# Kernel tuning notes

Hardware: AMD Instinct MI355X
Metric: run time of the kernel (lower is better)

Reference implementation:

```python
import jax, jax.numpy as jnp
import numpy as np
from jax.scipy.special import i0

# --- NUFFT adjoint (Kaiser-Bessel gridding) configuration ---
N = 512            # image side (image_shape)
K = 2 * N
M = 200_000        # n_measurements (visibilities)
B = 8              # batch of measurement vectors
J = 6              # gridding kernel width (plan uses (6, 6))
BETA = 2.34 * J


def setup_inputs() -> dict:
    key = jax.random.key(0)
    k1, k2, k3 = jax.random.split(key, 3)
    # uv coordinates in [-pi, pi) radians per pixel (standard NUFFT convention)
    uv = jax.random.uniform(k1, (M, 2), jnp.float32, -np.pi, np.pi)
    y_real = jax.random.normal(k2, (B, M), jnp.float32)
    y_imag = jax.random.normal(k3, (B, M), jnp.float32)
    weights = jnp.ones((M,), jnp.float32)  # measurement_weights
    return {"y_real": y_real, "y_imag": y_imag, "uv": uv, "weights": weights}


def _grid_1d(coord):
    """Per-axis gridding indices and Kaiser-Bessel weights.

    coord: (M,) frequencies in [-pi, pi). Returns idx (M, J) int32 grid
    columns (wrapped mod K) and w (M, J) float32 kernel weights.
    """
    k = coord / (2.0 * np.pi) * K            # grid units, in [-K/2, K/2)
    km = jnp.floor(k - J / 2.0)              # leftmost neighbor base
    j = jnp.arange(1, J + 1, dtype=k.dtype)
    pts = km[:, None] + j                    # (M, J) grid points covered
    d = k[:, None] - pts                     # signed distance, |d| <= J/2
    arg = jnp.maximum(1.0 - (2.0 * d / J) ** 2, 0.0)
    w = i0(BETA * jnp.sqrt(arg)) / i0(jnp.float32(BETA))
    idx = jnp.mod(pts, K).astype(jnp.int32)
    return idx, w.astype(jnp.float32)


def _deapod(n):
    """Gridding-correction (inverse FT of the KB kernel) at image pixels."""
    x = (jnp.arange(n, dtype=jnp.float32) - n / 2.0) / K
    t = BETA ** 2 - (np.pi * J * x) ** 2
    st = jnp.sqrt(jnp.abs(t))
    num = jnp.where(t > 0, jnp.sinh(st), jnp.sin(st))
    return num / jnp.maximum(st, 1e-6)


def reference(y_real, y_imag, uv, weights):
    y = (y_real + 1j * y_imag).astype(jnp.complex64) * weights  # (B, M)

    ix, wx = _grid_1d(uv[:, 0])  # (M, J)
    iy, wy = _grid_1d(uv[:, 1])  # (M, J)

    # Separable 6x6 kernel: outer products per measurement
    flat_idx = (ix[:, :, None] * K + iy[:, None, :]).reshape(-1)        # (M*J*J,)
    w2 = (wx[:, :, None] * wy[:, None, :]).reshape(M, J * J)            # (M, 36)
    vals = (y[:, :, None] * w2[None]).reshape(B, -1)                    # (B, M*36)

    # Scatter-add onto the oversampled grid (duplicate indices accumulate)
    grid = jnp.zeros((B, K * K), jnp.complex64).at[:, flat_idx].add(vals)
    grid = grid.reshape(B, K, K)

    # Unnormalized inverse FFT (adjoint of the forward FFT), shift to center
    img = jnp.fft.fftshift(jnp.fft.ifft2(grid), axes=(-2, -1)) * (K * K)

    # Crop central N x N region and de-apodize
    s = (K - N) // 2
    img_c = jnp.real(img[:, s:s + N, s:s + N])
    apod = _deapod(N)
    return img_c / (apod[:, None] * apod[None, :])
```

## Files before the change

### kernel.cpp

```cpp
#include <hip/hip_runtime.h>
#include <hip/hip_fp16.h>
#include <math.h>

#define KGRID 1024
#define NIMG  512
#define JW    6
#define BETAF 14.04f
#define NB    8
#define NBIN  16384
#define CAP   96

typedef float v2f __attribute__((ext_vector_type(2)));
typedef float v4f __attribute__((ext_vector_type(4)));

__device__ __forceinline__ float i0f_dev(float x) {
    float ax = fabsf(x);
    if (ax < 3.75f) {
        float z = ax * (1.0f / 3.75f);
        z = z * z;
        return 1.0f + z * (3.5156229f + z * (3.0899424f + z * (1.2067492f +
               z * (0.2659732f + z * (0.0360768f + z * 0.0045813f)))));
    } else {
        float z = 3.75f / ax;
        float p = 0.39894228f + z * (0.01328592f + z * (0.00225319f + z * (-0.00157565f +
                  z * (0.00916281f + z * (-0.02057706f + z * (0.02635537f +
                  z * (-0.01647633f + z * 0.00392377f)))))));
        return expf(ax) * rsqrtf(ax) * p;
    }
}

__global__ __launch_bounds__(256) void prep_kernel(
    const float* __restrict__ yr, const float* __restrict__ yi,
    const float* __restrict__ uv, const float* __restrict__ wts,
    float4* __restrict__ yF4, float4* __restrict__ pnt,
    int* __restrict__ cnt, int* __restrict__ list, int M)
{
    int m = (blockIdx.x >> 1) * 256 + threadIdx.x;
    if (m >= M) return;

    float u = uv[2 * m], v = uv[2 * m + 1];
    const float c2g = (float)KGRID / 6.283185307179586f;
    float kx = u * c2g, ky = v * c2g;
    float kmx = floorf(kx - 3.0f), kmy = floorf(ky - 3.0f);
    int x0m = (((int)kmx + 1) + 1024) & 1023;
    int y0m = (((int)kmy + 1) + 1024) & 1023;

    if ((blockIdx.x & 1) == 0) {
        int txA = x0m >> 3, txB = (txA + 1) & 127;
        int tyA = y0m >> 3, tyB = (tyA + 1) & 127;
        bool bx = (x0m & 7) >= 3;
        bool by = (y0m & 7) >= 3;
        int b0 = (txA << 7) | tyA;
        int b1 = (txA << 7) | tyB;
        int b2 = (txB << 7) | tyA;
        int b3 = (txB << 7) | tyB;
        int s0 = atomicAdd(&cnt[b0], 1);
        int s1 = by ? atomicAdd(&cnt[b1], 1) : -1;
        int s2 = bx ? atomicAdd(&cnt[b2], 1) : -1;
        int s3 = (bx && by) ? atomicAdd(&cnt[b3], 1) : -1;
        if ((unsigned)s0 < CAP) list[b0 * CAP + s0] = m;
        if ((unsigned)s1 < CAP) list[b1 * CAP + s1] = m;
        if ((unsigned)s2 < CAP) list[b2 * CAP + s2] = m;
        if ((unsigned)s3 < CAP) list[b3 * CAP + s3] = m;
    } else {
        if (m == 0) {
            float4 z = make_float4(0.f, 0.f, 0.f, 0.f);
            #pragma unroll
            for (int q = 0; q < 4; q++) { pnt[(size_t)M * 4 + q] = z; yF4[(size_t)M * 4 + q] = z; }
        }

        float inv = 1.0f / i0f_dev(BETAF);
        float s2c = inv * inv;
        float sc = wts[m] * s2c;

        float wx[JW], wy[JW];
        #pragma unroll
        for (int j = 0; j < JW; j++) {
            float dx = kx - kmx - 1.0f - (float)j;
            float rx = dx * (1.0f / 3.0f);
            float ax = fmaxf(1.0f - rx * rx, 0.0f);
            wx[j] = i0f_dev(BETAF * sqrtf(ax)) * sc;
            float dy = ky - kmy - 1.0f - (float)j;
            float ry = dy * (1.0f / 3.0f);
            float ay = fmaxf(1.0f - ry * ry, 0.0f);
            wy[j] = i0f_dev(BETAF * sqrtf(ay));
        }

        float4* p = pnt + (size_t)m * 4;
        p[0] = make_float4(wx[0], wx[1], wx[2], wx[3]);
        p[1] = make_float4(wx[4], wx[5], __int_as_float((x0m << 10) | y0m), 0.0f);
        p[2] = make_float4(wy[0], wy[1], wy[2], wy[3]);
        p[3] = make_float4(wy[4], wy[5], 0.0f, 0.0f);

        #pragma unroll
        for (int bp = 0; bp < 4; bp++) {
            int bb = 2 * bp;
            yF4[(size_t)m * 4 + bp] = make_float4(
                yr[(size_t)bb * M + m],       yi[(size_t)bb * M + m],
                yr[(size_t)(bb + 1) * M + m], yi[(size_t)(bb + 1) * M + m]);
        }
    }
}

__global__ __launch_bounds__(256) void grid_tile(
    const float* __restrict__ pnt1, const float4* __restrict__ yF4,
    const int* __restrict__ cnt, const int* __restrict__ list,
    __half2* __restrict__ gH, int M)
{
    int lane = threadIdx.x & 63;
    int wid  = threadIdx.x >> 6;
    int tile = blockIdx.x * 4 + wid;
    int tx0 = (tile >> 7) << 3;
    int ty0 = (tile & 127) << 3;
    int lx = lane >> 3, ly = lane & 7;
    int slot = lane & 15;

    v2f acc[NB];
    #pragma unroll
    for (int b = 0; b < NB; b++) acc[b] = (v2f){0.f, 0.f};

    int n = cnt[tile]; if (n > CAP) n = CAP;
    const int* lst = list + tile * CAP;
    const v4f* yV = (const v4f*)yF4;

    int lv0 = (lane < n) ? lst[lane] : M;
    int lv1 = (64 + lane < n && 64 + lane < CAP) ? lst[64 + lane] : M;

    #define FETCH_M(i) __builtin_amdgcn_readlane(((i) < 64) ? lv0 : lv1, (i) & 63)

    int   mA = FETCH_M(0), mB = FETCH_M(1), mC = FETCH_M(2);
    float pwA = pnt1[(size_t)mA * 16 + slot];
    float pwB = pnt1[(size_t)mB * 16 + slot];
    float pwC = pnt1[(size_t)mC * 16 + slot];
    v4f yA0 = yV[(size_t)mA * 4 + 0], yA1 = yV[(size_t)mA * 4 + 1],
        yA2 = yV[(size_t)mA * 4 + 2], yA3 = yV[(size_t)mA * 4 + 3];
    v4f yB0 = yV[(size_t)mB * 4 + 0], yB1 = yV[(size_t)mB * 4 + 1],
        yB2 = yV[(size_t)mB * 4 + 2], yB3 = yV[(size_t)mB * 4 + 3];
    v4f yC0 = yV[(size_t)mC * 4 + 0], yC1 = yV[(size_t)mC * 4 + 1],
        yC2 = yV[(size_t)mC * 4 + 2], yC3 = yV[(size_t)mC * 4 + 3];

    #define PROC(PW, Y0, Y1, Y2, Y3, IDX)                                          \
    {                                                                              \
        int mN = FETCH_M((IDX) + 3);                                               \
        int pwb = __float_as_int(PW);                                              \
        int meta = __builtin_amdgcn_readlane(pwb, 6);                              \
        int j1 = (tx0 + lx - (meta >> 10)) & 1023;                                 \
        int j2 = (ty0 + ly - (meta & 1023)) & 1023;                                 \
        int i1 = (j1 < 6) ? j1 : 15;                              \
        int i2 = (j2 < 6) ? (j2 + 8) : 14;                        \
        float wx = __int_as_float(__builtin_amdgcn_ds_bpermute(i1 << 2, pwb));     \
        float wy = __int_as_float(__builtin_amdgcn_ds_bpermute(i2 << 2, pwb));     \
        float w = wx * wy;                                                         \
        v2f w2 = {w, w};                                                           \
        acc[0] = __builtin_elementwise_fma(w2, Y0.xy, acc[0]);                     \
        acc[1] = __builtin_elementwise_fma(w2, Y0.zw, acc[1]);                     \
        acc[2] = __builtin_elementwise_fma(w2, Y1.xy, acc[2]);                     \
        acc[3] = __builtin_elementwise_fma(w2, Y1.zw, acc[3]);                     \
        acc[4] = __builtin_elementwise_fma(w2, Y2.xy, acc[4]);                     \
        acc[5] = __builtin_elementwise_fma(w2, Y2.zw, acc[5]);                     \
        acc[6] = __builtin_elementwise_fma(w2, Y3.xy, acc[6]);                     \
        acc[7] = __builtin_elementwise_fma(w2, Y3.zw, acc[7]);                     \
        PW = pnt1[(size_t)mN * 16 + slot];                                         \
        Y0 = yV[(size_t)mN * 4 + 0];                                               \
        Y1 = yV[(size_t)mN * 4 + 1];                                               \
        Y2 = yV[(size_t)mN * 4 + 2];                                               \
        Y3 = yV[(size_t)mN * 4 + 3];                                               \
    }

    for (int i = 0; i < n; i += 3) {
        PROC(pwA, yA0, yA1, yA2, yA3, i);
        PROC(pwB, yB0, yB1, yB2, yB3, i + 1);
        PROC(pwC, yC0, yC1, yC2, yC3, i + 2);
    }
    #undef PROC
    #undef FETCH_M

    size_t cell = ((size_t)(tx0 + lx) << 10) + (size_t)(ty0 + ly);
    #pragma unroll
    for (int b = 0; b < NB; b++)
        gH[((size_t)b << 20) + cell] = __float22half2_rn(make_float2(acc[b].x, acc[b].y));
}

#define SW(i) ((i) ^ (((i) >> 4) & 15))

__device__ __forceinline__ void fft1024_inv2(float2* X, float2* Y, const float2* W, int tid)
{
    float2* src = X;
    float2* dst = Y;
    #pragma unroll
    for (int stage = 0; stage < 5; stage++) {
        const int s = 1 << (2 * stage);
        __syncthreads();
        int t = tid;
        int a = t & ~(s - 1);
        float2 x0 = src[SW(t)];
        float2 x1 = src[SW(t + 256)];
        float2 x2 = src[SW(t + 512)];
        float2 x3 = src[SW(t + 768)];
        float2 u0 = src[SW(t) + 1024];
        float2 u1 = src[SW(t + 256) + 1024];
        float2 u2 = src[SW(t + 512) + 1024];
        float2 u3 = src[SW(t + 768) + 1024];
        float2 w1 = W[a];
        float2 w2 = W[2 * a];
        float2 w3 = make_float2(w1.x * w2.x - w1.y * w2.y,
                                w1.x * w2.y + w1.y * w2.x);
        int ob = 3 * a + t;
        {
            float2 d0 = make_float2(x0.x + x2.x, x0.y + x2.y);
            float2 e0 = make_float2(x0.x - x2.x, x0.y - x2.y);
            float2 d1 = make_float2(x1.x + x3.x, x1.y + x3.y);
            float2 e1 = make_float2(-(x1.y - x3.y), x1.x - x3.x);
            float2 s0 = make_float2(d0.x + d1.x, d0.y + d1.y);
            float2 s1 = make_float2(e0.x + e1.x, e0.y + e1.y);
            float2 s2 = make_float2(d0.x - d1.x, d0.y - d1.y);
            float2 s3 = make_float2(e0.x - e1.x, e0.y - e1.y);
            dst[SW(ob)]         = s0;
            dst[SW(ob + s)]     = make_float2(w1.x * s1.x - w1.y * s1.y,
                                              w1.x * s1.y + w1.y * s1.x);
            dst[SW(ob + 2 * s)] = make_float2(w2.x * s2.x - w2.y * s2.y,
                                              w2.x * s2.y + w2.y * s2.x);
            dst[SW(ob + 3 * s)] = make_float2(w3.x * s3.x - w3.y * s3.y,
                                              w3.x * s3.y + w3.y * s3.x);
        }
        {
            float2 d0 = make_float2(u0.x + u2.x, u0.y + u2.y);
            float2 e0 = make_float2(u0.x - u2.x, u0.y - u2.y);
            float2 d1 = make_float2(u1.x + u3.x, u1.y + u3.y);
            float2 e1 = make_float2(-(u1.y - u3.y), u1.x - u3.x);
            float2 s0 = make_float2(d0.x + d1.x, d0.y + d1.y);
            float2 s1 = make_float2(e0.x + e1.x, e0.y + e1.y);
            float2 s2 = make_float2(d0.x - d1.x, d0.y - d1.y);
            float2 s3 = make_float2(e0.x - e1.x, e0.y - e1.y);
            dst[SW(ob) + 1024]         = s0;
            dst[SW(ob + s) + 1024]     = make_float2(w1.x * s1.x - w1.y * s1.y,
                                                     w1.x * s1.y + w1.y * s1.x);
            dst[SW(ob + 2 * s) + 1024] = make_float2(w2.x * s2.x - w2.y * s2.y,
                                                     w2.x * s2.y + w2.y * s2.x);
            dst[SW(ob + 3 * s) + 1024] = make_float2(w3.x * s3.x - w3.y * s3.y,
                                                     w3.x * s3.y + w3.y * s3.x);
        }
        float2* tmp = src; src = dst; dst = tmp;
    }
    __syncthreads();
}

__global__ __launch_bounds__(256) void fft_pass1(const __half2* __restrict__ gH,
                                                 __half2* __restrict__ T)
{
    __shared__ float2 A[2048];
    __shared__ float2 Bb[2048];
    __shared__ float2 W[512];
    __shared__ __half2 R[8][512];

    int blk = blockIdx.x;
    int p   = blk >> 7;
    int g   = blk & 127;
    int tid = threadIdx.x;

    #pragma unroll
    for (int h = 0; h < 2; h++) {
        int j = tid + (h << 8);
        float sn, cn;
        __sincosf(6.283185307179586f * (float)j * (1.0f / 1024.0f), &sn, &cn);
        W[j] = make_float2(cn, sn);
    }

    const __half2* gA = gH + ((size_t)(2 * p)     << 20);
    const __half2* gB = gH + ((size_t)(2 * p + 1) << 20);

    for (int f = 0; f < 4; f++) {
        int k1a  = 4 * g + f;
        int k1b  = 1020 - 4 * g + f;
        int nk1a = (1024 - k1a) & 1023;
        int nk1b = (1024 - k1b) & 1023;
        const __half2* rAa  = gA + ((size_t)k1a  << 10);
        const __half2* rAan = gA + ((size_t)nk1a << 10);
        const __half2* rBa  = gB + ((size_t)k1a  << 10);
        const __half2* rBan = gB + ((size_t)nk1a << 10);
        const __half2* rAb  = gA + ((size_t)k1b  << 10);
        const __half2* rAbn = gA + ((size_t)nk1b << 10);
        const __half2* rBb  = gB + ((size_t)k1b  << 10);
        const __half2* rBbn = gB + ((size_t)nk1b << 10);
        __syncthreads();
        #pragma unroll
        for (int h = 0; h < 4; h++) {
            int k2  = tid + (h << 8);
            int nk2 = (1024 - k2) & 1023;
            float2 va  = __half22float2(rAa[k2]);
            float2 van = __half22float2(rAan[nk2]);
            float2 vb  = __half22float2(rBa[k2]);
            float2 vbn = __half22float2(rBan[nk2]);
            A[SW(k2)] = make_float2(0.5f * (va.x + van.x) - 0.5f * (vb.y - vbn.y),
                                    0.5f * (va.y - van.y) + 0.5f * (vb.x + vbn.x));
            float2 vc  = __half22float2(rAb[k2]);
            float2 vcn = __half22float2(rAbn[nk2]);
            float2 vd  = __half22float2(rBb[k2]);
            float2 vdn = __half22float2(rBbn[nk2]);
            A[SW(k2) + 1024] = make_float2(0.5f * (vc.x + vcn.x) - 0.5f * (vd.y - vdn.y),
                                           0.5f * (vc.y - vcn.y) + 0.5f * (vd.x + vdn.x));
        }
        fft1024_inv2(A, Bb, W, tid);
        #pragma unroll
        for (int h = 0; h < 2; h++) {
            int xo2 = tid + (h << 8);
            int sidx = SW((xo2 + 768) & 1023);
            R[f][xo2]     = __float22half2_rn(Bb[sidx]);
            R[f + 4][xo2] = __float22half2_rn(Bb[sidx + 1024]);
        }
    }
    __syncthreads();

    #pragma unroll
    for (int h = 0; h < 2; h++) {
        int xo2 = tid + (h << 8);
        __half2* Trow = T + (((size_t)p * 512 + xo2) << 10);
        int4 q0, q1;
        q0.x = *(const int*)&R[0][xo2]; q0.y = *(const int*)&R[1][xo2];
        q0.z = *(const int*)&R[2][xo2]; q0.w = *(const int*)&R[3][xo2];
        q1.x = *(const int*)&R[4][xo2]; q1.y = *(const int*)&R[5][xo2];
        q1.z = *(const int*)&R[6][xo2]; q1.w = *(const int*)&R[7][xo2];
        *(int4*)(Trow + 4 * g)          = q0;
        *(int4*)(Trow + (1020 - 4 * g)) = q1;
    }
}

__device__ __forceinline__ float apodf(int n) {
    float x  = ((float)n - 256.0f) * (1.0f / 1024.0f);
    float px = 3.14159265358979f * 6.0f * x;
    float t  = BETAF * BETAF - px * px;
    float st = sqrtf(fabsf(t));
    float num = (t > 0.0f) ? sinhf(st) : __sinf(st);
    return num / fmaxf(st, 1e-6f);
}

__global__ __launch_bounds__(256) void fft_pass2(const __half2* __restrict__ T,
                                                 float* __restrict__ out)
{
    __shared__ float2 A[2048];
    __shared__ float2 Bb[2048];
    __shared__ float2 W[512];
    __shared__ float2 R[4][512];

    int blk = blockIdx.x;
    int p   = blk >> 7;
    int xg  = blk & 127;
    int tid = threadIdx.x;

    #pragma unroll
    for (int h = 0; h < 2; h++) {
        int j = tid + (h << 8);
        float sn, cn;
        __sincosf(6.283185307179586f * (float)j * (1.0f / 1024.0f), &sn, &cn);
        W[j] = make_float2(cn, sn);
    }

    float a2[4];
    #pragma unroll
    for (int r = 0; r < 4; r++) a2[r] = apodf((xg << 2) + r);

    for (int r = 0; r < 2; r++) {
        int xo2a = (xg << 2) + 2 * r;
        int xo2b = xo2a + 1;
        const __half2* rowA = T + (((size_t)p * 512 + xo2a) << 10);
        const __half2* rowB = T + (((size_t)p * 512 + xo2b) << 10);
        __syncthreads();
        #pragma unroll
        for (int h = 0; h < 4; h++) {
            int i = tid + (h << 8);
            A[SW(i)]        = __half22float2(rowA[i]);
            A[SW(i) + 1024] = __half22float2(rowB[i]);
        }
        fft1024_inv2(A, Bb, W, tid);
        #pragma unroll
        for (int h = 0; h < 2; h++) {
            int xo1 = tid + (h << 8);
            int sidx = SW((xo1 + 768) & 1023);
            float2 v0 = Bb[sidx];
            float2 v1 = Bb[sidx + 1024];
            R[2 * r][xo1]     = make_float2(v0.x / a2[2 * r],     v0.y / a2[2 * r]);
            R[2 * r + 1][xo1] = make_float2(v1.x / a2[2 * r + 1], v1.y / a2[2 * r + 1]);
        }
    }
    __syncthreads();

    int b0 = 2 * p;
    #pragma unroll
    for (int h = 0; h < 2; h++) {
        int xo1 = tid + (h << 8);
        float inva1 = 1.0f / apodf(xo1);
        float2 f0 = R[0][xo1], f1 = R[1][xo1], f2 = R[2][xo1], f3 = R[3][xo1];
        float4* o0 = (float4*)(out + (((size_t)b0 * 512 + xo1) << 9) + (xg << 2));
        float4* o1 = (float4*)(out + (((size_t)(b0 + 1) * 512 + xo1) << 9) + (xg << 2));
        *o0 = make_float4(f0.x * inva1, f1.x * inva1, f2.x * inva1, f3.x * inva1);
        *o1 = make_float4(f0.y * inva1, f1.y * inva1, f2.y * inva1, f3.y * inva1);
    }
}

extern "C" void kernel_launch(void* const* d_in, const int* in_sizes, int n_in,
                              void* d_out, int out_size, void* d_ws, size_t ws_size,
                              hipStream_t stream)
{
    const float* yr  = (const float*)d_in[0];
    const float* yi  = (const float*)d_in[1];
    const float* uv  = (const float*)d_in[2];
    const float* wts = (const float*)d_in[3];

    int M = in_sizes[3];

    __half2* gH = (__half2*)d_ws;
    __half2* T  = (__half2*)((char*)d_ws + ((size_t)32 << 20));
    char*    p2 = (char*)d_ws + ((size_t)64 << 20);
    int*    cnt  = (int*)p2;
    int*    list = (int*)(p2 + 65536);
    float4* yF4  = (float4*)(p2 + 6553600);
    float4* pnt  = (float4*)(p2 + 19500032);

    hipMemsetAsync(cnt, 0, NBIN * sizeof(int), stream);
    int nb = (M + 255) / 256;
    prep_kernel<<<dim3(2 * nb), dim3(256), 0, stream>>>(
        yr, yi, uv, wts, yF4, pnt, cnt, list, M);
    grid_tile<<<dim3(NBIN / 4), dim3(256), 0, stream>>>(
        (const float*)pnt, (const float4*)yF4, cnt, list, gH, M);
    fft_pass1<<<dim3(4 * 128), dim3(256), 0, stream>>>(gH, T);
    fft_pass2<<<dim3(4 * 128), dim3(256), 0, stream>>>(T, (float*)d_out);
}
```

Before: 160.0 us.

## Store grid base offset in bin list and gather kernel weights per lane directly

The bin list now holds (measurement index, packed grid base) pairs, so grid_tile reads the base with readlane instead of pulling it from the per-point weight record. Each lane loads its own x and y weights straight from global memory at the computed index, which replaces the two ds_bpermute shuffles. The software pipeline also deepens from 3 to 4 in-flight measurements, with sched barriers separating the compute and refill phases. This removes the cross-lane shuffle latency in exchange for two scattered 4-byte loads per lane per point, more registers, and a relocated workspace layout.

```diff
diff --git a/kernel.cpp b/kernel.cpp
--- a/kernel.cpp
+++ b/kernel.cpp
@@ -33,7 +33,7 @@
     const float* __restrict__ yr, const float* __restrict__ yi,
     const float* __restrict__ uv, const float* __restrict__ wts,
     float4* __restrict__ yF4, float4* __restrict__ pnt,
-    int* __restrict__ cnt, int* __restrict__ list, int M)
+    int* __restrict__ cnt, int2* __restrict__ list, int M)
 {
     int m = (blockIdx.x >> 1) * 256 + threadIdx.x;
     if (m >= M) return;
@@ -46,6 +46,7 @@
     int y0m = (((int)kmy + 1) + 1024) & 1023;
 
     if ((blockIdx.x & 1) == 0) {
+        int meta = (x0m << 10) | y0m;
         int txA = x0m >> 3, txB = (txA + 1) & 127;
         int tyA = y0m >> 3, tyB = (tyA + 1) & 127;
         bool bx = (x0m & 7) >= 3;
@@ -58,10 +59,10 @@
         int s1 = by ? atomicAdd(&cnt[b1], 1) : -1;
         int s2 = bx ? atomicAdd(&cnt[b2], 1) : -1;
         int s3 = (bx && by) ? atomicAdd(&cnt[b3], 1) : -1;
-        if ((unsigned)s0 < CAP) list[b0 * CAP + s0] = m;
-        if ((unsigned)s1 < CAP) list[b1 * CAP + s1] = m;
-        if ((unsigned)s2 < CAP) list[b2 * CAP + s2] = m;
-        if ((unsigned)s3 < CAP) list[b3 * CAP + s3] = m;
+        if ((unsigned)s0 < CAP) list[b0 * CAP + s0] = make_int2(m, meta);
+        if ((unsigned)s1 < CAP) list[b1 * CAP + s1] = make_int2(m, meta);
+        if ((unsigned)s2 < CAP) list[b2 * CAP + s2] = make_int2(m, meta);
+        if ((unsigned)s3 < CAP) list[b3 * CAP + s3] = make_int2(m, meta);
     } else {
         if (m == 0) {
             float4 z = make_float4(0.f, 0.f, 0.f, 0.f);
@@ -88,7 +89,7 @@
 
         float4* p = pnt + (size_t)m * 4;
         p[0] = make_float4(wx[0], wx[1], wx[2], wx[3]);
-        p[1] = make_float4(wx[4], wx[5], __int_as_float((x0m << 10) | y0m), 0.0f);
+        p[1] = make_float4(wx[4], wx[5], 0.0f, 0.0f);
         p[2] = make_float4(wy[0], wy[1], wy[2], wy[3]);
         p[3] = make_float4(wy[4], wy[5], 0.0f, 0.0f);
 
@@ -104,7 +105,7 @@
 
 __global__ __launch_bounds__(256) void grid_tile(
     const float* __restrict__ pnt1, const float4* __restrict__ yF4,
-    const int* __restrict__ cnt, const int* __restrict__ list,
+    const int* __restrict__ cnt, const int2* __restrict__ list,
     __half2* __restrict__ gH, int M)
 {
     int lane = threadIdx.x & 63;
@@ -113,44 +114,44 @@
     int tx0 = (tile >> 7) << 3;
     int ty0 = (tile & 127) << 3;
     int lx = lane >> 3, ly = lane & 7;
-    int slot = lane & 15;
 
     v2f acc[NB];
     #pragma unroll
     for (int b = 0; b < NB; b++) acc[b] = (v2f){0.f, 0.f};
 
     int n = cnt[tile]; if (n > CAP) n = CAP;
-    const int* lst = list + tile * CAP;
+    const int2* lst = list + tile * CAP;
     const v4f* yV = (const v4f*)yF4;
 
-    int lv0 = (lane < n) ? lst[lane] : M;
-    int lv1 = (64 + lane < n && 64 + lane < CAP) ? lst[64 + lane] : M;
-
-    #define FETCH_M(i) __builtin_amdgcn_readlane(((i) < 64) ? lv0 : lv1, (i) & 63)
-
-    int   mA = FETCH_M(0), mB = FETCH_M(1), mC = FETCH_M(2);
-    float pwA = pnt1[(size_t)mA * 16 + slot];
-    float pwB = pnt1[(size_t)mB * 16 + slot];
-    float pwC = pnt1[(size_t)mC * 16 + slot];
-    v4f yA0 = yV[(size_t)mA * 4 + 0], yA1 = yV[(size_t)mA * 4 + 1],
-        yA2 = yV[(size_t)mA * 4 + 2], yA3 = yV[(size_t)mA * 4 + 3];
-    v4f yB0 = yV[(size_t)mB * 4 + 0], yB1 = yV[(size_t)mB * 4 + 1],
-        yB2 = yV[(size_t)mB * 4 + 2], yB3 = yV[(size_t)mB * 4 + 3];
-    v4f yC0 = yV[(size_t)mC * 4 + 0], yC1 = yV[(size_t)mC * 4 + 1],
-        yC2 = yV[(size_t)mC * 4 + 2], yC3 = yV[(size_t)mC * 4 + 3];
-
-    #define PROC(PW, Y0, Y1, Y2, Y3, IDX)                                          \
+    int2 lv0 = (lane < n) ? lst[lane] : make_int2(M, 0);
+    int2 lv1 = (64 + lane < n && 64 + lane < CAP) ? lst[64 + lane] : make_int2(M, 0);
+
+    #define GET_M(i)  __builtin_amdgcn_readlane(((i) < 64) ? lv0.x : lv1.x, (i) & 63)
+    #define GET_MT(i) __builtin_amdgcn_readlane(((i) < 64) ? lv0.y : lv1.y, (i) & 63)
+
+    float wxA, wyA, wxB, wyB, wxC, wyC, wxD, wyD;
+    v4f yA0, yA1, yA2, yA3, yB0, yB1, yB2, yB3;
+    v4f yC0, yC1, yC2, yC3, yD0, yD1, yD2, yD3;
+
+    #define REFILL(WX, WY, Y0, Y1, Y2, Y3, IDX)                                    \
     {                                                                              \
-        int mN = FETCH_M((IDX) + 3);                                               \
-        int pwb = __float_as_int(PW);                                              \
-        int meta = __builtin_amdgcn_readlane(pwb, 6);                              \
-        int j1 = (tx0 + lx - (meta >> 10)) & 1023;                                 \
-        int j2 = (ty0 + ly - (meta & 1023)) & 1023;                                 \
+        int mN = GET_M(IDX);                                                       \
+        int mt = GET_MT(IDX);                                                      \
+        int j1 = (tx0 + lx - (mt >> 10)) & 1023;                                   \
+        int j2 = (ty0 + ly - (mt & 1023)) & 1023;                                  \
         int i1 = (j1 < 6) ? j1 : 15;                              \
         int i2 = (j2 < 6) ? (j2 + 8) : 14;                        \
-        float wx = __int_as_float(__builtin_amdgcn_ds_bpermute(i1 << 2, pwb));     \
-        float wy = __int_as_float(__builtin_amdgcn_ds_bpermute(i2 << 2, pwb));     \
-        float w = wx * wy;                                                         \
+        WX = pnt1[((unsigned)mN << 4) + (unsigned)i1];                             \
+        WY = pnt1[((unsigned)mN << 4) + (unsigned)i2];                             \
+        Y0 = yV[(size_t)mN * 4 + 0];                                               \
+        Y1 = yV[(size_t)mN * 4 + 1];                                               \
+        Y2 = yV[(size_t)mN * 4 + 2];                                               \
+        Y3 = yV[(size_t)mN * 4 + 3];                                               \
+    }
+
+    #define USE(WX, WY, Y0, Y1, Y2, Y3)                                            \
+    {                                                                              \
+        float w = WX * WY;                                                         \
         v2f w2 = {w, w};                                                           \
         acc[0] = __builtin_elementwise_fma(w2, Y0.xy, acc[0]);                     \
         acc[1] = __builtin_elementwise_fma(w2, Y0.zw, acc[1]);                     \
@@ -160,20 +161,29 @@
         acc[5] = __builtin_elementwise_fma(w2, Y2.zw, acc[5]);                     \
         acc[6] = __builtin_elementwise_fma(w2, Y3.xy, acc[6]);                     \
         acc[7] = __builtin_elementwise_fma(w2, Y3.zw, acc[7]);                     \
-        PW = pnt1[(size_t)mN * 16 + slot];                                         \
-        Y0 = yV[(size_t)mN * 4 + 0];                                               \
-        Y1 = yV[(size_t)mN * 4 + 1];                                               \
-        Y2 = yV[(size_t)mN * 4 + 2];                                               \
-        Y3 = yV[(size_t)mN * 4 + 3];                                               \
-    }
-
-    for (int i = 0; i < n; i += 3) {
-        PROC(pwA, yA0, yA1, yA2, yA3, i);
-        PROC(pwB, yB0, yB1, yB2, yB3, i + 1);
-        PROC(pwC, yC0, yC1, yC2, yC3, i + 2);
-    }
-    #undef PROC
-    #undef FETCH_M
+    }
+
+    REFILL(wxA, wyA, yA0, yA1, yA2, yA3, 0);
+    REFILL(wxB, wyB, yB0, yB1, yB2, yB3, 1);
+    REFILL(wxC, wyC, yC0, yC1, yC2, yC3, 2);
+    REFILL(wxD, wyD, yD0, yD1, yD2, yD3, 3);
+
+    for (int i = 0; i < n; i += 4) {
+        USE(wxA, wyA, yA0, yA1, yA2, yA3);
+        USE(wxB, wyB, yB0, yB1, yB2, yB3);
+        USE(wxC, wyC, yC0, yC1, yC2, yC3);
+        USE(wxD, wyD, yD0, yD1, yD2, yD3);
+        __builtin_amdgcn_sched_barrier(0);
+        REFILL(wxA, wyA, yA0, yA1, yA2, yA3, i + 4);
+        REFILL(wxB, wyB, yB0, yB1, yB2, yB3, i + 5);
+        REFILL(wxC, wyC, yC0, yC1, yC2, yC3, i + 6);
+        REFILL(wxD, wyD, yD0, yD1, yD2, yD3, i + 7);
+        __builtin_amdgcn_sched_barrier(0);
+    }
+    #undef USE
+    #undef REFILL
+    #undef GET_M
+    #undef GET_MT
 
     size_t cell = ((size_t)(tx0 + lx) << 10) + (size_t)(ty0 + ly);
     #pragma unroll
@@ -410,11 +420,11 @@
 
     __half2* gH = (__half2*)d_ws;
     __half2* T  = (__half2*)((char*)d_ws + ((size_t)32 << 20));
+    int2*   list = (int2*)((char*)d_ws + ((size_t)40 << 20));
     char*    p2 = (char*)d_ws + ((size_t)64 << 20);
     int*    cnt  = (int*)p2;
-    int*    list = (int*)(p2 + 65536);
-    float4* yF4  = (float4*)(p2 + 6553600);
-    float4* pnt  = (float4*)(p2 + 19500032);
+    float4* yF4  = (float4*)(p2 + 65536);
+    float4* pnt  = (float4*)(p2 + 65536 + 12800064);
 
     hipMemsetAsync(cnt, 0, NBIN * sizeof(int), stream);
     int nb = (M + 255) / 256;
```

Result: slower. 165.3 us (+3.3%).

## Use in-place DIF radix-4 FFT with digit-reversed readout and double block count

Applied to the files above, without the earlier changes.

Replaces the ping-pong Stockham radix-4 FFT with an in-place decimation-in-frequency FFT whose output is read through a base-4 digit reversal. This removes the second 16 KB shared buffer, halves the twiddle table by computing w2 from w1, and shrinks the result staging arrays. Both FFT passes now do half the work per block and launch twice as many blocks, raising occupancy and parallelism. In exchange, pass1 no longer pairs symmetric rows, pass2 writes narrower float2 outputs, and the digit-reversed readout may cause more shared-memory bank conflicts.

```diff
diff --git a/kernel.cpp b/kernel.cpp
--- a/kernel.cpp
+++ b/kernel.cpp
@@ -183,64 +183,48 @@
 
 #define SW(i) ((i) ^ (((i) >> 4) & 15))
 
-__device__ __forceinline__ void fft1024_inv2(float2* X, float2* Y, const float2* W, int tid)
-{
-    float2* src = X;
-    float2* dst = Y;
-    #pragma unroll
-    for (int stage = 0; stage < 5; stage++) {
-        const int s = 1 << (2 * stage);
+__device__ __forceinline__ int dr4(int k) {
+    return ((k & 3) << 8) | ((k & 12) << 4) | (k & 48) | ((k >> 4) & 12) | ((k >> 8) & 3);
+}
+
+__device__ __forceinline__ void fft1024_dif2(float2* A, const float2* W, int tid)
+{
+    #pragma unroll
+    for (int s = 0; s < 5; s++) {
+        const int LQ = 8 - 2 * s;
         __syncthreads();
-        int t = tid;
-        int a = t & ~(s - 1);
-        float2 x0 = src[SW(t)];
-        float2 x1 = src[SW(t + 256)];
-        float2 x2 = src[SW(t + 512)];
-        float2 x3 = src[SW(t + 768)];
-        float2 u0 = src[SW(t) + 1024];
-        float2 u1 = src[SW(t + 256) + 1024];
-        float2 u2 = src[SW(t + 512) + 1024];
-        float2 u3 = src[SW(t + 768) + 1024];
+        int j    = tid & ((1 << LQ) - 1);
+        int base = ((tid >> LQ) << (LQ + 2)) + j;
+        int span = 1 << LQ;
+        int a    = j << (2 * s);
         float2 w1 = W[a];
-        float2 w2 = W[2 * a];
+        float2 w2 = make_float2(w1.x * w1.x - w1.y * w1.y, 2.0f * w1.x * w1.y);
         float2 w3 = make_float2(w1.x * w2.x - w1.y * w2.y,
                                 w1.x * w2.y + w1.y * w2.x);
-        int ob = 3 * a + t;
-        {
+        int i0 = SW(base);
+        int i1 = SW(base + span);
+        int i2 = SW(base + 2 * span);
+        int i3 = SW(base + 3 * span);
+        #pragma unroll
+        for (int r = 0; r < 2; r++) {
+            int o = r << 10;
+            float2 x0 = A[i0 + o], x1 = A[i1 + o], x2 = A[i2 + o], x3 = A[i3 + o];
             float2 d0 = make_float2(x0.x + x2.x, x0.y + x2.y);
             float2 e0 = make_float2(x0.x - x2.x, x0.y - x2.y);
             float2 d1 = make_float2(x1.x + x3.x, x1.y + x3.y);
             float2 e1 = make_float2(-(x1.y - x3.y), x1.x - x3.x);
-            float2 s0 = make_float2(d0.x + d1.x, d0.y + d1.y);
-            float2 s1 = make_float2(e0.x + e1.x, e0.y + e1.y);
-            float2 s2 = make_float2(d0.x - d1.x, d0.y - d1.y);
-            float2 s3 = make_float2(e0.x - e1.x, e0.y - e1.y);
-            dst[SW(ob)]         = s0;
-            dst[SW(ob + s)]     = make_float2(w1.x * s1.x - w1.y * s1.y,
-                                              w1.x * s1.y + w1.y * s1.x);
-            dst[SW(ob + 2 * s)] = make_float2(w2.x * s2.x - w2.y * s2.y,
-                                              w2.x * s2.y + w2.y * s2.x);
-            dst[SW(ob + 3 * s)] = make_float2(w3.x * s3.x - w3.y * s3.y,
-                                              w3.x * s3.y + w3.y * s3.x);
-        }
-        {
-            float2 d0 = make_float2(u0.x + u2.x, u0.y + u2.y);
-            float2 e0 = make_float2(u0.x - u2.x, u0.y - u2.y);
-            float2 d1 = make_float2(u1.x + u3.x, u1.y + u3.y);
-            float2 e1 = make_float2(-(u1.y - u3.y), u1.x - u3.x);
-            float2 s0 = make_float2(d0.x + d1.x, d0.y + d1.y);
-            float2 s1 = make_float2(e0.x + e1.x, e0.y + e1.y);
-            float2 s2 = make_float2(d0.x - d1.x, d0.y - d1.y);
-            float2 s3 = make_float2(e0.x - e1.x, e0.y - e1.y);
-            dst[SW(ob) + 1024]         = s0;
-            dst[SW(ob + s) + 1024]     = make_float2(w1.x * s1.x - w1.y * s1.y,
-                                                     w1.x * s1.y + w1.y * s1.x);
-            dst[SW(ob + 2 * s) + 1024] = make_float2(w2.x * s2.x - w2.y * s2.y,
-                                                     w2.x * s2.y + w2.y * s2.x);
-            dst[SW(ob + 3 * s) + 1024] = make_float2(w3.x * s3.x - w3.y * s3.y,
-                                                     w3.x * s3.y + w3.y * s3.x);
-        }
-        float2* tmp = src; src = dst; dst = tmp;
+            float2 g0 = make_float2(d0.x + d1.x, d0.y + d1.y);
+            float2 g1 = make_float2(e0.x + e1.x, e0.y + e1.y);
+            float2 g2 = make_float2(d0.x - d1.x, d0.y - d1.y);
+            float2 g3 = make_float2(e0.x - e1.x, e0.y - e1.y);
+            A[i0 + o] = g0;
+            A[i1 + o] = make_float2(w1.x * g1.x - w1.y * g1.y,
+                                    w1.x * g1.y + w1.y * g1.x);
+            A[i2 + o] = make_float2(w2.x * g2.x - w2.y * g2.y,
+                                    w2.x * g2.y + w2.y * g2.x);
+            A[i3 + o] = make_float2(w3.x * g3.x - w3.y * g3.y,
+                                    w3.x * g3.y + w3.y * g3.x);
+        }
     }
     __syncthreads();
 }
@@ -249,29 +233,26 @@
                                                  __half2* __restrict__ T)
 {
     __shared__ float2 A[2048];
-    __shared__ float2 Bb[2048];
-    __shared__ float2 W[512];
-    __shared__ __half2 R[8][512];
+    __shared__ float2 W[256];
+    __shared__ __half2 R[4][512];
 
     int blk = blockIdx.x;
-    int p   = blk >> 7;
-    int g   = blk & 127;
+    int p   = blk >> 8;
+    int g   = blk & 255;
     int tid = threadIdx.x;
 
-    #pragma unroll
-    for (int h = 0; h < 2; h++) {
-        int j = tid + (h << 8);
+    {
         float sn, cn;
-        __sincosf(6.283185307179586f * (float)j * (1.0f / 1024.0f), &sn, &cn);
-        W[j] = make_float2(cn, sn);
+        __sincosf(6.283185307179586f * (float)tid * (1.0f / 1024.0f), &sn, &cn);
+        W[tid] = make_float2(cn, sn);
     }
 
     const __half2* gA = gH + ((size_t)(2 * p)     << 20);
     const __half2* gB = gH + ((size_t)(2 * p + 1) << 20);
 
-    for (int f = 0; f < 4; f++) {
-        int k1a  = 4 * g + f;
-        int k1b  = 1020 - 4 * g + f;
+    for (int f = 0; f < 2; f++) {
+        int k1a  = 4 * g + 2 * f;
+        int k1b  = k1a + 1;
         int nk1a = (1024 - k1a) & 1023;
         int nk1b = (1024 - k1b) & 1023;
         const __half2* rAa  = gA + ((size_t)k1a  << 10);
@@ -300,13 +281,13 @@
             A[SW(k2) + 1024] = make_float2(0.5f * (vc.x + vcn.x) - 0.5f * (vd.y - vdn.y),
                                            0.5f * (vc.y - vcn.y) + 0.5f * (vd.x + vdn.x));
         }
-        fft1024_inv2(A, Bb, W, tid);
+        fft1024_dif2(A, W, tid);
         #pragma unroll
         for (int h = 0; h < 2; h++) {
             int xo2 = tid + (h << 8);
-            int sidx = SW((xo2 + 768) & 1023);
-            R[f][xo2]     = __float22half2_rn(Bb[sidx]);
-            R[f + 4][xo2] = __float22half2_rn(Bb[sidx + 1024]);
+            int q = dr4((xo2 + 768) & 1023);
+            R[2 * f][xo2]     = __float22half2_rn(A[SW(q)]);
+            R[2 * f + 1][xo2] = __float22half2_rn(A[SW(q) + 1024]);
         }
     }
     __syncthreads();
@@ -315,13 +296,10 @@
     for (int h = 0; h < 2; h++) {
         int xo2 = tid + (h << 8);
         __half2* Trow = T + (((size_t)p * 512 + xo2) << 10);
-        int4 q0, q1;
+        int4 q0;
         q0.x = *(const int*)&R[0][xo2]; q0.y = *(const int*)&R[1][xo2];
         q0.z = *(const int*)&R[2][xo2]; q0.w = *(const int*)&R[3][xo2];
-        q1.x = *(const int*)&R[4][xo2]; q1.y = *(const int*)&R[5][xo2];
-        q1.z = *(const int*)&R[6][xo2]; q1.w = *(const int*)&R[7][xo2];
-        *(int4*)(Trow + 4 * g)          = q0;
-        *(int4*)(Trow + (1020 - 4 * g)) = q1;
+        *(int4*)(Trow + 4 * g) = q0;
     }
 }
 
@@ -338,62 +316,46 @@
                                                  float* __restrict__ out)
 {
     __shared__ float2 A[2048];
-    __shared__ float2 Bb[2048];
-    __shared__ float2 W[512];
-    __shared__ float2 R[4][512];
+    __shared__ float2 W[256];
 
     int blk = blockIdx.x;
-    int p   = blk >> 7;
-    int xg  = blk & 127;
+    int p   = blk >> 8;
+    int xg  = blk & 255;
     int tid = threadIdx.x;
 
-    #pragma unroll
-    for (int h = 0; h < 2; h++) {
-        int j = tid + (h << 8);
+    {
         float sn, cn;
-        __sincosf(6.283185307179586f * (float)j * (1.0f / 1024.0f), &sn, &cn);
-        W[j] = make_float2(cn, sn);
-    }
-
-    float a2[4];
-    #pragma unroll
-    for (int r = 0; r < 4; r++) a2[r] = apodf((xg << 2) + r);
-
-    for (int r = 0; r < 2; r++) {
-        int xo2a = (xg << 2) + 2 * r;
-        int xo2b = xo2a + 1;
-        const __half2* rowA = T + (((size_t)p * 512 + xo2a) << 10);
-        const __half2* rowB = T + (((size_t)p * 512 + xo2b) << 10);
-        __syncthreads();
-        #pragma unroll
-        for (int h = 0; h < 4; h++) {
-            int i = tid + (h << 8);
-            A[SW(i)]        = __half22float2(rowA[i]);
-            A[SW(i) + 1024] = __half22float2(rowB[i]);
-        }
-        fft1024_inv2(A, Bb, W, tid);
-        #pragma unroll
-        for (int h = 0; h < 2; h++) {
-            int xo1 = tid + (h << 8);
-            int sidx = SW((xo1 + 768) & 1023);
-            float2 v0 = Bb[sidx];
-            float2 v1 = Bb[sidx + 1024];
-            R[2 * r][xo1]     = make_float2(v0.x / a2[2 * r],     v0.y / a2[2 * r]);
-            R[2 * r + 1][xo1] = make_float2(v1.x / a2[2 * r + 1], v1.y / a2[2 * r + 1]);
-        }
-    }
-    __syncthreads();
+        __sincosf(6.283185307179586f * (float)tid * (1.0f / 1024.0f), &sn, &cn);
+        W[tid] = make_float2(cn, sn);
+    }
+
+    float a2[2];
+    a2[0] = apodf(2 * xg);
+    a2[1] = apodf(2 * xg + 1);
+
+    const __half2* rowA = T + (((size_t)p * 512 + 2 * xg) << 10);
+    const __half2* rowB = rowA + 1024;
+    #pragma unroll
+    for (int h = 0; h < 4; h++) {
+        int i = tid + (h << 8);
+        A[SW(i)]        = __half22float2(rowA[i]);
+        A[SW(i) + 1024] = __half22float2(rowB[i]);
+    }
+    fft1024_dif2(A, W, tid);
 
     int b0 = 2 * p;
     #pragma unroll
     for (int h = 0; h < 2; h++) {
         int xo1 = tid + (h << 8);
+        int q = dr4((xo1 + 768) & 1023);
+        float2 v0 = A[SW(q)];
+        float2 v1 = A[SW(q) + 1024];
         float inva1 = 1.0f / apodf(xo1);
-        float2 f0 = R[0][xo1], f1 = R[1][xo1], f2 = R[2][xo1], f3 = R[3][xo1];
-        float4* o0 = (float4*)(out + (((size_t)b0 * 512 + xo1) << 9) + (xg << 2));
-        float4* o1 = (float4*)(out + (((size_t)(b0 + 1) * 512 + xo1) << 9) + (xg << 2));
-        *o0 = make_float4(f0.x * inva1, f1.x * inva1, f2.x * inva1, f3.x * inva1);
-        *o1 = make_float4(f0.y * inva1, f1.y * inva1, f2.y * inva1, f3.y * inva1);
+        float s0 = inva1 / a2[0], s1 = inva1 / a2[1];
+        float2* o0 = (float2*)(out + (((size_t)b0 * 512 + xo1) << 9) + (xg << 1));
+        float2* o1 = (float2*)(out + (((size_t)(b0 + 1) * 512 + xo1) << 9) + (xg << 1));
+        *o0 = make_float2(v0.x * s0, v1.x * s1);
+        *o1 = make_float2(v0.y * s0, v1.y * s1);
     }
 }
 
@@ -422,6 +384,6 @@
         yr, yi, uv, wts, yF4, pnt, cnt, list, M);
     grid_tile<<<dim3(NBIN / 4), dim3(256), 0, stream>>>(
         (const float*)pnt, (const float4*)yF4, cnt, list, gH, M);
-    fft_pass1<<<dim3(4 * 128), dim3(256), 0, stream>>>(gH, T);
-    fft_pass2<<<dim3(4 * 128), dim3(256), 0, stream>>>(T, (float*)d_out);
-}
+    fft_pass1<<<dim3(4 * 256), dim3(256), 0, stream>>>(gH, T);
+    fft_pass2<<<dim3(4 * 256), dim3(256), 0, stream>>>(T, (float*)d_out);
+}
```

Result: no change. 162.3 us (+1.5%).
